# Kernel tuning notes

Measured on AMD Instinct MI355X. Metric: run time of the kernel, lower is better.

## Reference

```python
import jax, jax.numpy as jnp
import numpy as np

NUM_HEADS = 8
NUM_LEVEL = 4
KERNEL = 2
NUM_POINT = KERNEL * KERNEL
D_MODEL = 256
HEAD_DIM = D_MODEL // NUM_HEADS
REF_SIZE = 4
EPS = 1e-6


def _kernel_indices():
    # even kernel: linspace(-k/2+0.5, k/2-0.5, k) -> [-0.5, 0.5] for k=2
    ind = np.linspace(-KERNEL // 2 + 0.5, KERNEL // 2 - 0.5, KERNEL)
    i, j = np.meshgrid(ind, ind, indexing='ij')
    ki = np.stack([j, i], axis=-1).reshape(-1, 2) / KERNEL  # (P, 2), (x, y)
    return jnp.asarray(ki, dtype=jnp.float32)


def _ref_windows(shapes):
    # mask is None -> centers on a regular grid, size = ref_size / (H, W)
    refs = []
    for (H, W) in shapes:
        y = (jnp.arange(1, H + 1, dtype=jnp.float32) - 0.5) / (H + EPS)
        x = (jnp.arange(1, W + 1, dtype=jnp.float32) - 0.5) / (W + EPS)
        yy, xx = jnp.meshgrid(y, x, indexing='ij')           # (H, W)
        center = jnp.stack([xx, yy], axis=-1).reshape(-1, 2)  # (HW, 2)
        size = jnp.broadcast_to(
            jnp.array([REF_SIZE / W, REF_SIZE / H], dtype=jnp.float32), center.shape)
        refs.append(jnp.concatenate([center, size], axis=-1))
    return jnp.concatenate(refs, axis=0)  # (L, 4)


def _bilinear_sample(vflat, grid, H, W):
    """vflat: (B, H*W, M, D) one level; grid: (B, Lq, M, P, 2) normalized [0,1].
    Returns (B, Lq, M, P, D). Zero padding outside, align_corners=False."""
    B, _, M, D = vflat.shape
    x = grid[..., 0] * W - 0.5
    y = grid[..., 1] * H - 0.5
    x0 = jnp.floor(x); y0 = jnp.floor(y)
    lx = x - x0; ly = y - y0
    x0i = x0.astype(jnp.int32); y0i = y0.astype(jnp.int32)
    bidx = jnp.arange(B)[:, None, None, None]
    midx = jnp.arange(M)[None, None, :, None]

    def corner(xi, yi, w):
        valid = (xi >= 0) & (xi < W) & (yi >= 0) & (yi < H)
        idx = jnp.clip(yi, 0, H - 1) * W + jnp.clip(xi, 0, W - 1)
        g = vflat[bidx, idx, midx]  # (B, Lq, M, P, D)
        return g * (w * valid.astype(w.dtype))[..., None]

    out = corner(x0i, y0i, (1 - lx) * (1 - ly))
    out = out + corner(x0i + 1, y0i, lx * (1 - ly))
    out = out + corner(x0i, y0i + 1, (1 - lx) * ly)
    out = out + corner(x0i + 1, y0i + 1, lx * ly)
    return out


def setup_inputs() -> dict:
    key = jax.random.key(0)
    ks = jax.random.split(key, 20)
    spatial = [(100, 100), (50, 50), (25, 25), (13, 13)]
    B = 4
    inp = {}
    for i, (H, W) in enumerate(spatial):
        inp[f'value{i}'] = jax.random.normal(ks[i], (B, D_MODEL, H, W), dtype=jnp.float32)
        inp[f'pos{i}'] = jax.random.normal(ks[4 + i], (B, D_MODEL, H, W), dtype=jnp.float32)
    s = 0.05
    inp['Wv'] = jax.random.normal(ks[8], (D_MODEL, D_MODEL), dtype=jnp.float32) * s
    inp['bv'] = jnp.zeros((D_MODEL,), dtype=jnp.float32)
    inp['Wo'] = jax.random.normal(ks[9], (D_MODEL, D_MODEL), dtype=jnp.float32) * s
    inp['bo'] = jnp.zeros((D_MODEL,), dtype=jnp.float32)
    nb = NUM_LEVEL * NUM_HEADS * 4
    inp['Wbox'] = jax.random.normal(ks[10], (nb, D_MODEL), dtype=jnp.float32) * s
    inp['bbox'] = jax.random.uniform(ks[11], (nb,), dtype=jnp.float32)
    na = NUM_HEADS * NUM_LEVEL * NUM_POINT
    inp['Wattn'] = jax.random.normal(ks[12], (na, D_MODEL), dtype=jnp.float32) * s
    inp['battn'] = jax.random.normal(ks[13], (na,), dtype=jnp.float32) * s
    return inp


def reference(value0, value1, value2, value3, pos0, pos1, pos2, pos3,
              Wv, bv, Wo, bo, Wbox, bbox, Wattn, battn):
    levels = [value0, value1, value2, value3]
    poss = [pos0, pos1, pos2, pos3]
    shapes = [(v.shape[2], v.shape[3]) for v in levels]
    B = levels[0].shape[0]

    # flatten pyramid: (B, C, H, W) -> (B, HW, C)
    value = jnp.concatenate(
        [v.reshape(B, D_MODEL, -1).transpose(0, 2, 1) for v in levels], axis=1)
    pos = jnp.concatenate(
        [p.reshape(B, D_MODEL, -1).transpose(0, 2, 1) for p in poss], axis=1)
    L = value.shape[1]

    query = value + pos
    vp = (value @ Wv.T + bv).reshape(B, L, NUM_HEADS, HEAD_DIM)

    attn = jax.nn.softmax(
        (query @ Wattn.T + battn).reshape(B, L, NUM_HEADS, NUM_LEVEL * NUM_POINT),
        axis=-1).reshape(B, L, NUM_HEADS, NUM_LEVEL, NUM_POINT)

    offset = (query @ Wbox.T + bbox).reshape(B, L, NUM_HEADS, NUM_LEVEL, 4)
    ref = _ref_windows(shapes)[None, :, None, None, :]          # (1, L, 1, 1, 4)
    boxes = ref + offset / 8.0 * ref[..., jnp.array([2, 3, 2, 3])]
    center = boxes[..., None, :2]                               # (B, L, M, NL, 1, 2)
    size = boxes[..., None, 2:]
    ki = _kernel_indices()[None, None, None, None, :, :]        # (1,1,1,1,P,2)
    grid = center + ki * jax.nn.relu(size)                      # (B, L, M, NL, P, 2)

    out = jnp.zeros((B, L, NUM_HEADS, HEAD_DIM), dtype=vp.dtype)
    start = 0
    for l, (H, W) in enumerate(shapes):
        end = start + H * W
        vf = vp[:, start:end]                                   # (B, HW, M, D)
        sampled = _bilinear_sample(vf, grid[:, :, :, l], H, W)  # (B, L, M, P, D)
        out = out + jnp.einsum('blmp,blmpd->blmd', attn[:, :, :, l], sampled)
        start = end

    return out.reshape(B, L, D_MODEL) @ Wo.T + bo
```

## Files before the change

kernel.cpp:

```cpp
#include <hip/hip_runtime.h>
#include <cstdint>
#include <cmath>

#define D_MODEL 256
#define NH 8
#define NLVL 4
#define LTOT 13294
#define BATCH 4
#define BTOT (BATCH * LTOT)
#define RPAD 53248

typedef __attribute__((ext_vector_type(8))) short bf8;
typedef __attribute__((ext_vector_type(4))) float f4;

__device__ __forceinline__ unsigned short f2bf(float x) {
    unsigned u = __float_as_uint(x);
    u += 0x7fffu + ((u >> 16) & 1u);
    return (unsigned short)(u >> 16);
}
__device__ __forceinline__ float bf2f(unsigned short h) {
    return __uint_as_float(((unsigned)h) << 16);
}
__device__ __forceinline__ int swzf(int i, int s) { return s ^ ((i >> 1) & 3); }

__device__ __forceinline__ void level_of(int l, int& lv, int& hw, int& Wl, int& HWl, int& loff) {
    if (l < 10000)      { lv = 0; loff = 0;     Wl = 100; HWl = 10000; }
    else if (l < 12500) { lv = 1; loff = 10000; Wl = 50;  HWl = 2500;  }
    else if (l < 13125) { lv = 2; loff = 12500; Wl = 25;  HWl = 625;   }
    else                { lv = 3; loff = 13125; Wl = 13;  HWl = 169;   }
    hw = l - loff;
}

__global__ __launch_bounds__(256) void pack_weights(
    const float* __restrict__ Wv, const float* __restrict__ Wattn,
    const float* __restrict__ Wbox, const float* __restrict__ Wo,
    unsigned short* __restrict__ W1hi, unsigned short* __restrict__ W1lo,
    unsigned short* __restrict__ Wohi, unsigned short* __restrict__ Wolo) {
    int tid = blockIdx.x * 256 + threadIdx.x;
    const float* src;
    unsigned short *dh, *dl;
    int nb, kb, j, s;
    if (tid < 16384) {
        nb = tid >> 12; kb = (tid >> 9) & 7; j = (tid >> 2) & 127; s = tid & 3;
        int f = nb * 128 + j, c0 = kb * 32 + s * 8;
        if (f < 256)      src = Wv + (size_t)f * 256 + c0;
        else if (f < 384) src = Wattn + (size_t)(f - 256) * 256 + c0;
        else              src = Wbox + (size_t)(f - 384) * 256 + c0;
        dh = W1hi; dl = W1lo;
    } else if (tid < 24576) {
        int t2 = tid - 16384;
        nb = t2 >> 12; kb = (t2 >> 9) & 7; j = (t2 >> 2) & 127; s = t2 & 3;
        int f = nb * 128 + j, c0 = kb * 32 + s * 8;
        src = Wo + (size_t)f * 256 + c0;
        dh = Wohi; dl = Wolo;
    } else return;
    int base = (((nb * 8 + kb) * 128 + j) * 4 + swzf(j, s)) * 8;
    #pragma unroll
    for (int e = 0; e < 8; ++e) {
        float x = src[e];
        unsigned short h = f2bf(x);
        dh[base + e] = h;
        dl[base + e] = f2bf(x - bf2f(h));
    }
}

__global__ __launch_bounds__(256) void convert_A(
    const float* __restrict__ v0, const float* __restrict__ v1,
    const float* __restrict__ v2, const float* __restrict__ v3,
    const float* __restrict__ p0, const float* __restrict__ p1,
    const float* __restrict__ p2, const float* __restrict__ p3,
    unsigned short* __restrict__ Gv, unsigned short* __restrict__ Gq) {
    __shared__ unsigned short HV[64][130];
    __shared__ unsigned short HQ[64][130];
    int t = threadIdx.x;
    int w = t >> 6, lane = t & 63;
    int r0 = blockIdx.x * 64;

    int r = r0 + lane; if (r >= BTOT) r = BTOT - 1;
    int b = r / LTOT, l = r % LTOT;
    int lv, hw, Wl, HWl, loff;
    level_of(l, lv, hw, Wl, HWl, loff);
    const float *vb, *pb;
    switch (lv) { case 0: vb = v0; pb = p0; break; case 1: vb = v1; pb = p1; break;
                  case 2: vb = v2; pb = p2; break; default: vb = v3; pb = p3; break; }
    size_t base = (size_t)b * D_MODEL * (size_t)HWl + (size_t)hw;
    vb += base; pb += base;

    int kb2 = (lane >> 2) & 3, slot = lane & 3;
    for (int h = 0; h < 2; ++h) {
        #pragma unroll 4
        for (int i = 0; i < 32; ++i) {
            int cl = i * 4 + w;
            int c = h * 128 + cl;
            float av = vb[(size_t)c * HWl];
            float aq = av + pb[(size_t)c * HWl];
            HV[lane][cl] = f2bf(av);
            HQ[lane][cl] = f2bf(aq);
        }
        __syncthreads();
        #pragma unroll
        for (int j = 0; j < 8; ++j) {
            int plane = j >> 2;
            int rl = (j & 3) * 16 + w * 4 + (lane >> 4);
            int oct = slot ^ ((rl >> 1) & 3);
            const unsigned* s32 = (const unsigned*)(plane ? &HQ[rl][kb2 * 32 + oct * 8]
                                                          : &HV[rl][kb2 * 32 + oct * 8]);
            uint4 vst = make_uint4(s32[0], s32[1], s32[2], s32[3]);
            unsigned short* dst = (plane ? Gq : Gv)
                + (size_t)(r0 + rl) * 256 + (h * 4 + kb2) * 32 + slot * 8;
            *(uint4*)dst = vst;
        }
        __syncthreads();
    }
}

__global__ __launch_bounds__(256) void gemm1_mfma(
    const unsigned short* __restrict__ Gv, const unsigned short* __restrict__ Gq,
    const unsigned short* __restrict__ W1hi, const unsigned short* __restrict__ W1lo,
    const float* __restrict__ bv, const float* __restrict__ battn, const float* __restrict__ bbox,
    unsigned short* __restrict__ VPb, float* __restrict__ LB) {
    __shared__ __align__(16) unsigned short Ah[4096], Bh[4096], Bl[4096];
    int t = threadIdx.x;
    int nb = blockIdx.x;
    int r0 = blockIdx.y * 128;
    const unsigned short* Asrc = (nb < 2) ? Gv : Gq;
    int w = t >> 6, lane = t & 63;
    int wr = w >> 1, wc = w & 1;
    int row_l = lane & 15, oct = lane >> 4;

    const unsigned short* Bbh = W1hi + (size_t)nb * 32768;
    const unsigned short* Bbl = W1lo + (size_t)nb * 32768;

    f4 acc[4][4];
    #pragma unroll
    for (int i = 0; i < 4; ++i)
        #pragma unroll
        for (int j = 0; j < 4; ++j) acc[i][j] = (f4){0.f, 0.f, 0.f, 0.f};

    int c0 = w * 64 + lane, c1 = c0 + 256;
    for (int kb = 0; kb < 8; ++kb) {
        __syncthreads();
        {
            const unsigned short* a0 = Asrc + (size_t)(r0 + (c0 >> 2)) * 256 + kb * 32 + (c0 & 3) * 8;
            const unsigned short* a1 = Asrc + (size_t)(r0 + (c1 >> 2)) * 256 + kb * 32 + (c1 & 3) * 8;
            __builtin_amdgcn_global_load_lds(a0, &Ah[w * 512], 16, 0, 0);
            __builtin_amdgcn_global_load_lds(a1, &Ah[2048 + w * 512], 16, 0, 0);
            const unsigned short* b0 = Bbh + kb * 4096 + c0 * 8;
            const unsigned short* b1 = Bbh + kb * 4096 + c1 * 8;
            __builtin_amdgcn_global_load_lds(b0, &Bh[w * 512], 16, 0, 0);
            __builtin_amdgcn_global_load_lds(b1, &Bh[2048 + w * 512], 16, 0, 0);
            const unsigned short* b2 = Bbl + kb * 4096 + c0 * 8;
            const unsigned short* b3 = Bbl + kb * 4096 + c1 * 8;
            __builtin_amdgcn_global_load_lds(b2, &Bl[w * 512], 16, 0, 0);
            __builtin_amdgcn_global_load_lds(b3, &Bl[2048 + w * 512], 16, 0, 0);
        }
        __syncthreads();
        bf8 a[4], bh[4], bl[4];
        #pragma unroll
        for (int x = 0; x < 4; ++x) {
            int ri = wr * 64 + x * 16 + row_l;
            int ci = wc * 64 + x * 16 + row_l;
            a[x]  = *(const bf8*)(&Ah[ri * 32 + swzf(ri, oct) * 8]);
            bh[x] = *(const bf8*)(&Bh[ci * 32 + swzf(ci, oct) * 8]);
            bl[x] = *(const bf8*)(&Bl[ci * 32 + swzf(ci, oct) * 8]);
        }
        #pragma unroll
        for (int mi = 0; mi < 4; ++mi)
            #pragma unroll
            for (int ni = 0; ni < 4; ++ni) {
                f4 c = acc[mi][ni];
                c = __builtin_amdgcn_mfma_f32_16x16x32_bf16(a[mi], bh[ni], c, 0, 0, 0);
                c = __builtin_amdgcn_mfma_f32_16x16x32_bf16(a[mi], bl[ni], c, 0, 0, 0);
                acc[mi][ni] = c;
            }
    }
    #pragma unroll
    for (int ni = 0; ni < 4; ++ni) {
        int col = wc * 64 + ni * 16 + row_l;
        float bias;
        if (nb == 0) bias = bv[col];
        else if (nb == 1) bias = bv[128 + col];
        else if (nb == 2) bias = battn[col];
        else bias = bbox[col];
        #pragma unroll
        for (int mi = 0; mi < 4; ++mi) {
            #pragma unroll
            for (int v = 0; v < 4; ++v) {
                int rr = r0 + wr * 64 + mi * 16 + oct * 4 + v;
                if (rr < BTOT) {
                    float val = acc[mi][ni][v] + bias;
                    if (nb < 2) VPb[(size_t)rr * 256 + nb * 128 + col] = f2bf(val);
                    else        LB[(size_t)rr * 256 + (nb - 2) * 128 + col] = val;
                }
            }
        }
    }
}

__global__ __launch_bounds__(256) void sampler_kernel(const unsigned short* __restrict__ VPb,
                                                      const float* __restrict__ LB,
                                                      unsigned short* __restrict__ att_hi,
                                                      unsigned short* __restrict__ att_lo) {
    __shared__ float sw[16][17][8];
    const int Ws2[4]   = {100, 50, 25, 13};
    const int offs2[4] = {0, 10000, 12500, 13125};
    int t = threadIdx.x;
    int blk = blockIdx.x;

    {
        int g = t >> 4, p = t & 15;
        int grp = blk * 16 + g;
        int m = grp & 7;
        int r = grp >> 3;
        int l = r % LTOT;
        int rb0 = r - l;

        int lv, hw, Wl, HWl, loff;
        level_of(l, lv, hw, Wl, HWl, loff);
        int x, y;
        switch (lv) {
            case 0:  y = hw / 100; x = hw - y * 100; break;
            case 1:  y = hw / 50;  x = hw - y * 50;  break;
            case 2:  y = hw / 25;  x = hw - y * 25;  break;
            default: y = hw / 13;  x = hw - y * 13;  break;
        }
        float denom = (float)((double)Wl + 1e-6);
        float cx = ((float)x + 0.5f) / denom;
        float cy = ((float)y + 0.5f) / denom;
        float rsw = 4.0f / (float)Wl;

        const float* Lrow = LB + (size_t)r * 256;
        float lg = Lrow[m * 16 + p];
        float mx = lg;
        #pragma unroll
        for (int off = 8; off >= 1; off >>= 1)
            mx = fmaxf(mx, __shfl_xor(mx, off, 16));
        float e = __expf(lg - mx);
        float ssum = e;
        #pragma unroll
        for (int off = 8; off >= 1; off >>= 1)
            ssum += __shfl_xor(ssum, off, 16);
        float aw = e / ssum;

        int lp = p >> 2, pp = p & 3;
        int W2 = Ws2[lp];
        float fW2 = (float)W2;
        float o0 = Lrow[128 + m * 16 + lp * 4 + 0];
        float o1 = Lrow[128 + m * 16 + lp * 4 + 1];
        float o2 = Lrow[128 + m * 16 + lp * 4 + 2];
        float o3 = Lrow[128 + m * 16 + lp * 4 + 3];
        float bcx = cx + o0 * 0.125f * rsw;
        float bcy = cy + o1 * 0.125f * rsw;
        float bsx = fmaxf(fmaf(o2 * 0.125f, rsw, rsw), 0.f);
        float bsy = fmaxf(fmaf(o3 * 0.125f, rsw, rsw), 0.f);
        float kx = (pp & 1)  ? 0.25f : -0.25f;
        float ky = (pp >> 1) ? 0.25f : -0.25f;
        float xs = fmaf(bcx + kx * bsx, fW2, -0.5f);
        float ys = fmaf(bcy + ky * bsy, fW2, -0.5f);
        float x0f = floorf(xs), y0f = floorf(ys);
        float lx = xs - x0f, ly = ys - y0f;
        int x0 = (int)x0f, y0 = (int)y0f;
        int x1 = x0 + 1, y1 = y0 + 1;
        bool vx0 = (x0 >= 0) & (x0 < W2), vx1 = (x1 >= 0) & (x1 < W2);
        bool vy0 = (y0 >= 0) & (y0 < W2), vy1 = (y1 >= 0) & (y1 < W2);
        int x0c = min(max(x0, 0), W2 - 1), x1c = min(max(x1, 0), W2 - 1);
        int y0c = min(max(y0, 0), W2 - 1), y1c = min(max(y1, 0), W2 - 1);
        float w00 = (vx0 & vy0) ? aw * (1.f - lx) * (1.f - ly) : 0.f;
        float w01 = (vx1 & vy0) ? aw * lx * (1.f - ly) : 0.f;
        float w10 = (vx0 & vy1) ? aw * (1.f - lx) * ly : 0.f;
        float w11 = (vx1 & vy1) ? aw * lx * ly : 0.f;
        int rowb = rb0 + offs2[lp];
        int col  = m * 32;
        int i00 = ((rowb + y0c * W2 + x0c) * 256 + col) * 2;
        int i01 = ((rowb + y0c * W2 + x1c) * 256 + col) * 2;
        int i10 = ((rowb + y1c * W2 + x0c) * 256 + col) * 2;
        int i11 = ((rowb + y1c * W2 + x1c) * 256 + col) * 2;
        sw[g][p][0] = w00; sw[g][p][1] = w01; sw[g][p][2] = w10; sw[g][p][3] = w11;
        sw[g][p][4] = __int_as_float(i00); sw[g][p][5] = __int_as_float(i01);
        sw[g][p][6] = __int_as_float(i10); sw[g][p][7] = __int_as_float(i11);
    }
    __syncthreads();

    int g = t >> 4, lane16 = t & 15;
    unsigned dby = (unsigned)lane16 * 4u;
    const char* Vb = (const char*)VPb;
    float acc0 = 0.f, acc1 = 0.f;
    #pragma unroll
    for (int p = 0; p < 16; ++p) {
        float4 w  = *(const float4*)&sw[g][p][0];
        float4 fi = *(const float4*)&sw[g][p][4];
        unsigned u0 = *(const unsigned*)(Vb + (size_t)(__float_as_uint(fi.x) + dby));
        unsigned u1 = *(const unsigned*)(Vb + (size_t)(__float_as_uint(fi.y) + dby));
        unsigned u2 = *(const unsigned*)(Vb + (size_t)(__float_as_uint(fi.z) + dby));
        unsigned u3 = *(const unsigned*)(Vb + (size_t)(__float_as_uint(fi.w) + dby));
        acc0 = fmaf(w.x, __uint_as_float(u0 << 16), acc0);
        acc1 = fmaf(w.x, __uint_as_float(u0 & 0xffff0000u), acc1);
        acc0 = fmaf(w.y, __uint_as_float(u1 << 16), acc0);
        acc1 = fmaf(w.y, __uint_as_float(u1 & 0xffff0000u), acc1);
        acc0 = fmaf(w.z, __uint_as_float(u2 << 16), acc0);
        acc1 = fmaf(w.z, __uint_as_float(u2 & 0xffff0000u), acc1);
        acc0 = fmaf(w.w, __uint_as_float(u3 << 16), acc0);
        acc1 = fmaf(w.w, __uint_as_float(u3 & 0xffff0000u), acc1);
    }
    int grp = blk * 16 + g;
    int m2 = grp & 7, r2 = grp >> 3;
    int d0 = lane16 * 2;
    unsigned short h0 = f2bf(acc0), h1 = f2bf(acc1);
    unsigned short l0 = f2bf(acc0 - bf2f(h0)), l1 = f2bf(acc1 - bf2f(h1));
    size_t base = (size_t)r2 * 256 + m2 * 32 + (((d0 >> 3) ^ ((r2 >> 1) & 3)) << 3) + (d0 & 7);
    *(unsigned*)&att_hi[base] = ((unsigned)h1 << 16) | (unsigned)h0;
    *(unsigned*)&att_lo[base] = ((unsigned)l1 << 16) | (unsigned)l0;
}

__global__ __launch_bounds__(256) void gemm2_mfma(
    const unsigned short* __restrict__ Ahi_g, const unsigned short* __restrict__ Alo_g,
    const unsigned short* __restrict__ Wohi, const unsigned short* __restrict__ Wolo,
    const float* __restrict__ bo, float* __restrict__ out) {
    __shared__ __align__(16) unsigned short Ah[4096], Al[4096], Bh[4096], Bl[4096];
    int t = threadIdx.x;
    int nb = blockIdx.x;
    int r0 = blockIdx.y * 128;
    int w = t >> 6, lane = t & 63;
    int wr = w >> 1, wc = w & 1;
    int row_l = lane & 15, oct = lane >> 4;

    const unsigned short* Bbh = Wohi + (size_t)nb * 32768;
    const unsigned short* Bbl = Wolo + (size_t)nb * 32768;

    f4 acc[4][4];
    #pragma unroll
    for (int i = 0; i < 4; ++i)
        #pragma unroll
        for (int j = 0; j < 4; ++j) acc[i][j] = (f4){0.f, 0.f, 0.f, 0.f};

    int c0 = w * 64 + lane, c1 = c0 + 256;
    int ra0 = r0 + (c0 >> 2); if (ra0 >= BTOT) ra0 = BTOT - 1;
    int ra1 = r0 + (c1 >> 2); if (ra1 >= BTOT) ra1 = BTOT - 1;
    for (int kb = 0; kb < 8; ++kb) {
        __syncthreads();
        {
            size_t s0 = (size_t)ra0 * 256 + kb * 32 + (c0 & 3) * 8;
            size_t s1 = (size_t)ra1 * 256 + kb * 32 + (c1 & 3) * 8;
            __builtin_amdgcn_global_load_lds(Ahi_g + s0, &Ah[w * 512], 16, 0, 0);
            __builtin_amdgcn_global_load_lds(Ahi_g + s1, &Ah[2048 + w * 512], 16, 0, 0);
            __builtin_amdgcn_global_load_lds(Alo_g + s0, &Al[w * 512], 16, 0, 0);
            __builtin_amdgcn_global_load_lds(Alo_g + s1, &Al[2048 + w * 512], 16, 0, 0);
            __builtin_amdgcn_global_load_lds(Bbh + kb * 4096 + c0 * 8, &Bh[w * 512], 16, 0, 0);
            __builtin_amdgcn_global_load_lds(Bbh + kb * 4096 + c1 * 8, &Bh[2048 + w * 512], 16, 0, 0);
            __builtin_amdgcn_global_load_lds(Bbl + kb * 4096 + c0 * 8, &Bl[w * 512], 16, 0, 0);
            __builtin_amdgcn_global_load_lds(Bbl + kb * 4096 + c1 * 8, &Bl[2048 + w * 512], 16, 0, 0);
        }
        __syncthreads();
        bf8 ah[4], al[4], bh[4], bl[4];
        #pragma unroll
        for (int x = 0; x < 4; ++x) {
            int ri = wr * 64 + x * 16 + row_l;
            int ci = wc * 64 + x * 16 + row_l;
            ah[x] = *(const bf8*)(&Ah[ri * 32 + swzf(ri, oct) * 8]);
            al[x] = *(const bf8*)(&Al[ri * 32 + swzf(ri, oct) * 8]);
            bh[x] = *(const bf8*)(&Bh[ci * 32 + swzf(ci, oct) * 8]);
            bl[x] = *(const bf8*)(&Bl[ci * 32 + swzf(ci, oct) * 8]);
        }
        #pragma unroll
        for (int mi = 0; mi < 4; ++mi)
            #pragma unroll
            for (int ni = 0; ni < 4; ++ni) {
                f4 c = acc[mi][ni];
                c = __builtin_amdgcn_mfma_f32_16x16x32_bf16(ah[mi], bh[ni], c, 0, 0, 0);
                c = __builtin_amdgcn_mfma_f32_16x16x32_bf16(ah[mi], bl[ni], c, 0, 0, 0);
                c = __builtin_amdgcn_mfma_f32_16x16x32_bf16(al[mi], bh[ni], c, 0, 0, 0);
                acc[mi][ni] = c;
            }
    }
    #pragma unroll
    for (int ni = 0; ni < 4; ++ni) {
        int col = wc * 64 + ni * 16 + row_l;
        float bias = bo[nb * 128 + col];
        #pragma unroll
        for (int mi = 0; mi < 4; ++mi) {
            #pragma unroll
            for (int v = 0; v < 4; ++v) {
                int rr = r0 + wr * 64 + mi * 16 + oct * 4 + v;
                if (rr < BTOT)
                    out[(size_t)rr * 256 + nb * 128 + col] = acc[mi][ni][v] + bias;
            }
        }
    }
}

extern "C" void kernel_launch(void* const* d_in, const int* in_sizes, int n_in,
                              void* d_out, int out_size, void* d_ws, size_t ws_size,
                              hipStream_t stream) {
    const float* v0 = (const float*)d_in[0];
    const float* p0 = (const float*)d_in[1];
    const float* v1 = (const float*)d_in[2];
    const float* p1 = (const float*)d_in[3];
    const float* v2 = (const float*)d_in[4];
    const float* p2 = (const float*)d_in[5];
    const float* v3 = (const float*)d_in[6];
    const float* p3 = (const float*)d_in[7];
    const float* Wv    = (const float*)d_in[8];
    const float* bv    = (const float*)d_in[9];
    const float* Wo    = (const float*)d_in[10];
    const float* bo    = (const float*)d_in[11];
    const float* Wbox  = (const float*)d_in[12];
    const float* bbox  = (const float*)d_in[13];
    const float* Wattn = (const float*)d_in[14];
    const float* battn = (const float*)d_in[15];
    float* out = (float*)d_out;

    char* ws = (char*)d_ws;
    unsigned short* W1hi = (unsigned short*)(ws);
    unsigned short* W1lo = (unsigned short*)(ws + 262144);
    unsigned short* Wohi = (unsigned short*)(ws + 524288);
    unsigned short* Wolo = (unsigned short*)(ws + 655360);
    unsigned short* Gv   = (unsigned short*)(ws + 1048576);
    unsigned short* Gq   = (unsigned short*)(ws + 1048576 + 27262976);
    unsigned short* atth = Gv;
    unsigned short* attl = Gq;
    unsigned short* VPb  = (unsigned short*)(ws + 1048576 + 2 * 27262976);
    float*          LB   = (float*)(ws + 1048576 + 2 * 27262976 + 27226112);

    convert_A<<<dim3(RPAD / 64), dim3(256), 0, stream>>>(v0, v1, v2, v3,
                                                         p0, p1, p2, p3, Gv, Gq);
    pack_weights<<<dim3(96), dim3(256), 0, stream>>>(Wv, Wattn, Wbox, Wo,
                                                     W1hi, W1lo, Wohi, Wolo);

    gemm1_mfma<<<dim3(4, RPAD / 128), dim3(256), 0, stream>>>(
        Gv, Gq, W1hi, W1lo, bv, battn, bbox, VPb, LB);

    sampler_kernel<<<dim3((BTOT * NH) / 16), dim3(256), 0, stream>>>(VPb, LB, atth, attl);

    gemm2_mfma<<<dim3(2, (BTOT + 127) / 128), dim3(256), 0, stream>>>(
        atth, attl, Wohi, Wolo, bo, out);
}
```

Baseline: 251.3 us.

## Double-buffer GEMM LDS tiles and use packed FMA in sampler

```diff
diff --git a/kernel.cpp b/kernel.cpp
--- a/kernel.cpp
+++ b/kernel.cpp
@@ -12,6 +12,7 @@
 
 typedef __attribute__((ext_vector_type(8))) short bf8;
 typedef __attribute__((ext_vector_type(4))) float f4;
+typedef __attribute__((ext_vector_type(2))) float f2;
 
 __device__ __forceinline__ unsigned short f2bf(float x) {
     unsigned u = __float_as_uint(x);
@@ -119,7 +120,7 @@
     const unsigned short* __restrict__ W1hi, const unsigned short* __restrict__ W1lo,
     const float* __restrict__ bv, const float* __restrict__ battn, const float* __restrict__ bbox,
     unsigned short* __restrict__ VPb, float* __restrict__ LB) {
-    __shared__ __align__(16) unsigned short Ah[4096], Bh[4096], Bl[4096];
+    __shared__ __align__(16) unsigned short Ah[2][4096], Bh[2][4096], Bl[2][4096];
     int t = threadIdx.x;
     int nb = blockIdx.x;
     int r0 = blockIdx.y * 128;
@@ -138,31 +139,32 @@
         for (int j = 0; j < 4; ++j) acc[i][j] = (f4){0.f, 0.f, 0.f, 0.f};
 
     int c0 = w * 64 + lane, c1 = c0 + 256;
+    const unsigned short* a0b = Asrc + (size_t)(r0 + (c0 >> 2)) * 256 + (c0 & 3) * 8;
+    const unsigned short* a1b = Asrc + (size_t)(r0 + (c1 >> 2)) * 256 + (c1 & 3) * 8;
+
+#define G1_STAGE(bb, kb)                                                            \
+    {                                                                               \
+        __builtin_amdgcn_global_load_lds(a0b + (kb) * 32, &Ah[bb][w * 512], 16, 0, 0);        \
+        __builtin_amdgcn_global_load_lds(a1b + (kb) * 32, &Ah[bb][2048 + w * 512], 16, 0, 0); \
+        __builtin_amdgcn_global_load_lds(Bbh + (kb) * 4096 + c0 * 8, &Bh[bb][w * 512], 16, 0, 0);        \
+        __builtin_amdgcn_global_load_lds(Bbh + (kb) * 4096 + c1 * 8, &Bh[bb][2048 + w * 512], 16, 0, 0); \
+        __builtin_amdgcn_global_load_lds(Bbl + (kb) * 4096 + c0 * 8, &Bl[bb][w * 512], 16, 0, 0);        \
+        __builtin_amdgcn_global_load_lds(Bbl + (kb) * 4096 + c1 * 8, &Bl[bb][2048 + w * 512], 16, 0, 0); \
+    }
+
+    G1_STAGE(0, 0);
     for (int kb = 0; kb < 8; ++kb) {
         __syncthreads();
-        {
-            const unsigned short* a0 = Asrc + (size_t)(r0 + (c0 >> 2)) * 256 + kb * 32 + (c0 & 3) * 8;
-            const unsigned short* a1 = Asrc + (size_t)(r0 + (c1 >> 2)) * 256 + kb * 32 + (c1 & 3) * 8;
-            __builtin_amdgcn_global_load_lds(a0, &Ah[w * 512], 16, 0, 0);
-            __builtin_amdgcn_global_load_lds(a1, &Ah[2048 + w * 512], 16, 0, 0);
-            const unsigned short* b0 = Bbh + kb * 4096 + c0 * 8;
-            const unsigned short* b1 = Bbh + kb * 4096 + c1 * 8;
-            __builtin_amdgcn_global_load_lds(b0, &Bh[w * 512], 16, 0, 0);
-            __builtin_amdgcn_global_load_lds(b1, &Bh[2048 + w * 512], 16, 0, 0);
-            const unsigned short* b2 = Bbl + kb * 4096 + c0 * 8;
-            const unsigned short* b3 = Bbl + kb * 4096 + c1 * 8;
-            __builtin_amdgcn_global_load_lds(b2, &Bl[w * 512], 16, 0, 0);
-            __builtin_amdgcn_global_load_lds(b3, &Bl[2048 + w * 512], 16, 0, 0);
-        }
-        __syncthreads();
+        if (kb < 7) G1_STAGE((kb + 1) & 1, kb + 1);
+        int bb = kb & 1;
         bf8 a[4], bh[4], bl[4];
         #pragma unroll
         for (int x = 0; x < 4; ++x) {
             int ri = wr * 64 + x * 16 + row_l;
             int ci = wc * 64 + x * 16 + row_l;
-            a[x]  = *(const bf8*)(&Ah[ri * 32 + swzf(ri, oct) * 8]);
-            bh[x] = *(const bf8*)(&Bh[ci * 32 + swzf(ci, oct) * 8]);
-            bl[x] = *(const bf8*)(&Bl[ci * 32 + swzf(ci, oct) * 8]);
+            a[x]  = *(const bf8*)(&Ah[bb][ri * 32 + swzf(ri, oct) * 8]);
+            bh[x] = *(const bf8*)(&Bh[bb][ci * 32 + swzf(ci, oct) * 8]);
+            bl[x] = *(const bf8*)(&Bl[bb][ci * 32 + swzf(ci, oct) * 8]);
         }
         #pragma unroll
         for (int mi = 0; mi < 4; ++mi)
@@ -201,7 +203,7 @@
                                                       const float* __restrict__ LB,
                                                       unsigned short* __restrict__ att_hi,
                                                       unsigned short* __restrict__ att_lo) {
-    __shared__ float sw[16][17][8];
+    __shared__ float sw[16][260];
     const int Ws2[4]   = {100, 50, 25, 13};
     const int offs2[4] = {0, 10000, 12500, 13125};
     int t = threadIdx.x;
@@ -275,38 +277,42 @@
         int i01 = ((rowb + y0c * W2 + x1c) * 256 + col) * 2;
         int i10 = ((rowb + y1c * W2 + x0c) * 256 + col) * 2;
         int i11 = ((rowb + y1c * W2 + x1c) * 256 + col) * 2;
-        sw[g][p][0] = w00; sw[g][p][1] = w01; sw[g][p][2] = w10; sw[g][p][3] = w11;
-        sw[g][p][4] = __int_as_float(i00); sw[g][p][5] = __int_as_float(i01);
-        sw[g][p][6] = __int_as_float(i10); sw[g][p][7] = __int_as_float(i11);
+        float* dst = &sw[g][p * 16];
+        dst[0] = w00; dst[1] = w00; dst[2] = w01; dst[3] = w01;
+        dst[4] = w10; dst[5] = w10; dst[6] = w11; dst[7] = w11;
+        dst[8]  = __int_as_float(i00); dst[9]  = __int_as_float(i01);
+        dst[10] = __int_as_float(i10); dst[11] = __int_as_float(i11);
     }
     __syncthreads();
 
     int g = t >> 4, lane16 = t & 15;
     unsigned dby = (unsigned)lane16 * 4u;
     const char* Vb = (const char*)VPb;
-    float acc0 = 0.f, acc1 = 0.f;
+    f2 acc2 = {0.f, 0.f};
     #pragma unroll
     for (int p = 0; p < 16; ++p) {
-        float4 w  = *(const float4*)&sw[g][p][0];
-        float4 fi = *(const float4*)&sw[g][p][4];
+        const float* sp = &sw[g][p * 16];
+        float4 wA = *(const float4*)sp;
+        float4 wB = *(const float4*)(sp + 4);
+        float4 fi = *(const float4*)(sp + 8);
         unsigned u0 = *(const unsigned*)(Vb + (size_t)(__float_as_uint(fi.x) + dby));
         unsigned u1 = *(const unsigned*)(Vb + (size_t)(__float_as_uint(fi.y) + dby));
         unsigned u2 = *(const unsigned*)(Vb + (size_t)(__float_as_uint(fi.z) + dby));
         unsigned u3 = *(const unsigned*)(Vb + (size_t)(__float_as_uint(fi.w) + dby));
-        acc0 = fmaf(w.x, __uint_as_float(u0 << 16), acc0);
-        acc1 = fmaf(w.x, __uint_as_float(u0 & 0xffff0000u), acc1);
-        acc0 = fmaf(w.y, __uint_as_float(u1 << 16), acc0);
-        acc1 = fmaf(w.y, __uint_as_float(u1 & 0xffff0000u), acc1);
-        acc0 = fmaf(w.z, __uint_as_float(u2 << 16), acc0);
-        acc1 = fmaf(w.z, __uint_as_float(u2 & 0xffff0000u), acc1);
-        acc0 = fmaf(w.w, __uint_as_float(u3 << 16), acc0);
-        acc1 = fmaf(w.w, __uint_as_float(u3 & 0xffff0000u), acc1);
+        f2 v00 = {__uint_as_float(u0 << 16), __uint_as_float(u0 & 0xffff0000u)};
+        f2 v01 = {__uint_as_float(u1 << 16), __uint_as_float(u1 & 0xffff0000u)};
+        f2 v10 = {__uint_as_float(u2 << 16), __uint_as_float(u2 & 0xffff0000u)};
+        f2 v11 = {__uint_as_float(u3 << 16), __uint_as_float(u3 & 0xffff0000u)};
+        acc2 = __builtin_elementwise_fma((f2){wA.x, wA.y}, v00, acc2);
+        acc2 = __builtin_elementwise_fma((f2){wA.z, wA.w}, v01, acc2);
+        acc2 = __builtin_elementwise_fma((f2){wB.x, wB.y}, v10, acc2);
+        acc2 = __builtin_elementwise_fma((f2){wB.z, wB.w}, v11, acc2);
     }
     int grp = blk * 16 + g;
     int m2 = grp & 7, r2 = grp >> 3;
     int d0 = lane16 * 2;
-    unsigned short h0 = f2bf(acc0), h1 = f2bf(acc1);
-    unsigned short l0 = f2bf(acc0 - bf2f(h0)), l1 = f2bf(acc1 - bf2f(h1));
+    unsigned short h0 = f2bf(acc2.x), h1 = f2bf(acc2.y);
+    unsigned short l0 = f2bf(acc2.x - bf2f(h0)), l1 = f2bf(acc2.y - bf2f(h1));
     size_t base = (size_t)r2 * 256 + m2 * 32 + (((d0 >> 3) ^ ((r2 >> 1) & 3)) << 3) + (d0 & 7);
     *(unsigned*)&att_hi[base] = ((unsigned)h1 << 16) | (unsigned)h0;
     *(unsigned*)&att_lo[base] = ((unsigned)l1 << 16) | (unsigned)l0;
@@ -316,7 +322,7 @@
     const unsigned short* __restrict__ Ahi_g, const unsigned short* __restrict__ Alo_g,
     const unsigned short* __restrict__ Wohi, const unsigned short* __restrict__ Wolo,
     const float* __restrict__ bo, float* __restrict__ out) {
-    __shared__ __align__(16) unsigned short Ah[4096], Al[4096], Bh[4096], Bl[4096];
+    __shared__ __align__(16) unsigned short Ah[2][4096], Al[2][4096], Bh[2][4096], Bl[2][4096];
     int t = threadIdx.x;
     int nb = blockIdx.x;
     int r0 = blockIdx.y * 128;
@@ -336,30 +342,37 @@
     int c0 = w * 64 + lane, c1 = c0 + 256;
     int ra0 = r0 + (c0 >> 2); if (ra0 >= BTOT) ra0 = BTOT - 1;
     int ra1 = r0 + (c1 >> 2); if (ra1 >= BTOT) ra1 = BTOT - 1;
+    const unsigned short* ah0 = Ahi_g + (size_t)ra0 * 256 + (c0 & 3) * 8;
+    const unsigned short* ah1 = Ahi_g + (size_t)ra1 * 256 + (c1 & 3) * 8;
+    const unsigned short* al0 = Alo_g + (size_t)ra0 * 256 + (c0 & 3) * 8;
+    const unsigned short* al1 = Alo_g + (size_t)ra1 * 256 + (c1 & 3) * 8;
+
+#define G2_STAGE(bb, kb)                                                            \
+    {                                                                               \
+        __builtin_amdgcn_global_load_lds(ah0 + (kb) * 32, &Ah[bb][w * 512], 16, 0, 0);        \
+        __builtin_amdgcn_global_load_lds(ah1 + (kb) * 32, &Ah[bb][2048 + w * 512], 16, 0, 0); \
+        __builtin_amdgcn_global_load_lds(al0 + (kb) * 32, &Al[bb][w * 512], 16, 0, 0);        \
+        __builtin_amdgcn_global_load_lds(al1 + (kb) * 32, &Al[bb][2048 + w * 512], 16, 0, 0); \
+        __builtin_amdgcn_global_load_lds(Bbh + (kb) * 4096 + c0 * 8, &Bh[bb][w * 512], 16, 0, 0);        \
+        __builtin_amdgcn_global_load_lds(Bbh + (kb) * 4096 + c1 * 8, &Bh[bb][2048 + w * 512], 16, 0, 0); \
+        __builtin_amdgcn_global_load_lds(Bbl + (kb) * 4096 + c0 * 8, &Bl[bb][w * 512], 16, 0, 0);        \
+        __builtin_amdgcn_global_load_lds(Bbl + (kb) * 4096 + c1 * 8, &Bl[bb][2048 + w * 512], 16, 0, 0); \
+    }
+
+    G2_STAGE(0, 0);
     for (int kb = 0; kb < 8; ++kb) {
         __syncthreads();
-        {
-            size_t s0 = (size_t)ra0 * 256 + kb * 32 + (c0 & 3) * 8;
-            size_t s1 = (size_t)ra1 * 256 + kb * 32 + (c1 & 3) * 8;
-            __builtin_amdgcn_global_load_lds(Ahi_g + s0, &Ah[w * 512], 16, 0, 0);
-            __builtin_amdgcn_global_load_lds(Ahi_g + s1, &Ah[2048 + w * 512], 16, 0, 0);
-            __builtin_amdgcn_global_load_lds(Alo_g + s0, &Al[w * 512], 16, 0, 0);
-            __builtin_amdgcn_global_load_lds(Alo_g + s1, &Al[2048 + w * 512], 16, 0, 0);
-            __builtin_amdgcn_global_load_lds(Bbh + kb * 4096 + c0 * 8, &Bh[w * 512], 16, 0, 0);
-            __builtin_amdgcn_global_load_lds(Bbh + kb * 4096 + c1 * 8, &Bh[2048 + w * 512], 16, 0, 0);
-            __builtin_amdgcn_global_load_lds(Bbl + kb * 4096 + c0 * 8, &Bl[w * 512], 16, 0, 0);
-            __builtin_amdgcn_global_load_lds(Bbl + kb * 4096 + c1 * 8, &Bl[2048 + w * 512], 16, 0, 0);
-        }
-        __syncthreads();
+        if (kb < 7) G2_STAGE((kb + 1) & 1, kb + 1);
+        int bb = kb & 1;
         bf8 ah[4], al[4], bh[4], bl[4];
         #pragma unroll
         for (int x = 0; x < 4; ++x) {
             int ri = wr * 64 + x * 16 + row_l;
             int ci = wc * 64 + x * 16 + row_l;
-            ah[x] = *(const bf8*)(&Ah[ri * 32 + swzf(ri, oct) * 8]);
-            al[x] = *(const bf8*)(&Al[ri * 32 + swzf(ri, oct) * 8]);
-            bh[x] = *(const bf8*)(&Bh[ci * 32 + swzf(ci, oct) * 8]);
-            bl[x] = *(const bf8*)(&Bl[ci * 32 + swzf(ci, oct) * 8]);
+            ah[x] = *(const bf8*)(&Ah[bb][ri * 32 + swzf(ri, oct) * 8]);
+            al[x] = *(const bf8*)(&Al[bb][ri * 32 + swzf(ri, oct) * 8]);
+            bh[x] = *(const bf8*)(&Bh[bb][ci * 32 + swzf(ci, oct) * 8]);
+            bl[x] = *(const bf8*)(&Bl[bb][ci * 32 + swzf(ci, oct) * 8]);
         }
         #pragma unroll
         for (int mi = 0; mi < 4; ++mi)
```

Result: faster. 245.5 us (-2.3%).
